# Optimization experiments

Hardware: AMD Instinct MI355X
Metric: run time of the kernel (lower is better)

## Reference

```python
import jax, jax.numpy as jnp
import numpy as np

NUM_HEADS = 16
D_K = 64
D_V = 64
D_MODEL = 1024


def setup_inputs() -> dict:
    key = jax.random.key(0)
    ks = jax.random.split(key, 11)
    B, S = 2, 2048
    s = 0.02
    return {
        "Q": jax.random.normal(ks[0], (B, S, D_MODEL), jnp.float32),
        "K": jax.random.normal(ks[1], (B, S, D_MODEL), jnp.float32),
        "V": jax.random.normal(ks[2], (B, S, D_MODEL), jnp.float32),
        "WQ": jax.random.normal(ks[3], (D_MODEL, NUM_HEADS * D_K), jnp.float32) * s,
        "bQ": jnp.zeros((NUM_HEADS * D_K,), jnp.float32),
        "WK": jax.random.normal(ks[4], (D_MODEL, NUM_HEADS * D_K), jnp.float32) * s,
        "bK": jnp.zeros((NUM_HEADS * D_K,), jnp.float32),
        "WV": jax.random.normal(ks[5], (D_MODEL, NUM_HEADS * D_V), jnp.float32) * s,
        "bV": jnp.zeros((NUM_HEADS * D_V,), jnp.float32),
        "WO": jax.random.normal(ks[6], (NUM_HEADS * D_V, D_MODEL), jnp.float32) * s,
        "bO": jnp.zeros((D_MODEL,), jnp.float32),
    }


def reference(Q, K, V, WQ, bQ, WK, bK, WV, bV, WO, bO):
    B = Q.shape[0]
    # linear projections, then split heads: [B, H, S, d]
    q = (Q @ WQ + bQ).reshape(B, -1, NUM_HEADS, D_K).transpose(0, 2, 1, 3)
    k = (K @ WK + bK).reshape(B, -1, NUM_HEADS, D_K).transpose(0, 2, 1, 3)
    v = (V @ WV + bV).reshape(B, -1, NUM_HEADS, D_V).transpose(0, 2, 1, 3)
    # unfused attention: full [B, H, Sq, Sk] score matrix
    scores = jnp.einsum("bhqd,bhkd->bhqk", q, k) / jnp.sqrt(jnp.float32(D_K))
    attn = jax.nn.softmax(scores, axis=-1)  # dropout is identity in eval mode
    out = jnp.einsum("bhqk,bhkd->bhqd", attn, v)
    out = out.transpose(0, 2, 1, 3).reshape(B, -1, NUM_HEADS * D_V)
    return out @ WO + bO
```

## Files before the change

### kernel.cpp

```cpp
#include <hip/hip_runtime.h>
#include <hip/hip_bf16.h>
#include <stdint.h>

#define BATCH 2
#define SEQ   2048
#define NH    16
#define DH    64
#define DM    1024
#define MR    (BATCH * SEQ)

typedef __bf16 bf16_t;
typedef bf16_t bf16x4 __attribute__((ext_vector_type(4)));
typedef bf16_t bf16x8 __attribute__((ext_vector_type(8)));
typedef float  f32x4  __attribute__((ext_vector_type(4)));

typedef const __attribute__((address_space(1))) void* gas_t;
typedef       __attribute__((address_space(3))) void* las_t;

__device__ __forceinline__ void gload16(const void* g, void* l) {
  __builtin_amdgcn_global_load_lds((gas_t)g, (las_t)l, 16, 0, 0);
}

__device__ __forceinline__ float fast_exp2(float x) {
#if __has_builtin(__builtin_amdgcn_exp2f)
  return __builtin_amdgcn_exp2f(x);
#else
  float r; asm volatile("v_exp_f32 %0, %1\n\ts_nop 1" : "=v"(r) : "v"(x)); return r;
#endif
}

__global__ __launch_bounds__(256) void cvt3_kernel(const float* __restrict__ x0,
                                                   const float* __restrict__ x1,
                                                   const float* __restrict__ x2,
                                                   bf16_t* __restrict__ y0,
                                                   bf16_t* __restrict__ y1,
                                                   bf16_t* __restrict__ y2, int n) {
  const int z = blockIdx.y;
  const float* x = z == 0 ? x0 : (z == 1 ? x1 : x2);
  bf16_t*      y = z == 0 ? y0 : (z == 1 ? y1 : y2);
  int i = (blockIdx.x * 256 + threadIdx.x) * 8;
  if (i + 8 <= n) {
    float4 a = *(const float4*)(x + i);
    float4 b = *(const float4*)(x + i + 4);
    bf16x8 o;
    o[0] = (bf16_t)a.x; o[1] = (bf16_t)a.y; o[2] = (bf16_t)a.z; o[3] = (bf16_t)a.w;
    o[4] = (bf16_t)b.x; o[5] = (bf16_t)b.y; o[6] = (bf16_t)b.z; o[7] = (bf16_t)b.w;
    *(bf16x8*)(y + i) = o;
  }
}

__global__ __launch_bounds__(256) void wtrans4_kernel(const float* __restrict__ W0,
                                                      const float* __restrict__ W1,
                                                      const float* __restrict__ W2,
                                                      const float* __restrict__ W3,
                                                      bf16_t* __restrict__ T0,
                                                      bf16_t* __restrict__ T1,
                                                      bf16_t* __restrict__ T2,
                                                      bf16_t* __restrict__ T3) {
  const int z = blockIdx.z;
  const float* W = z == 0 ? W0 : (z == 1 ? W1 : (z == 2 ? W2 : W3));
  bf16_t*     Wt = z == 0 ? T0 : (z == 1 ? T1 : (z == 2 ? T2 : T3));
  __shared__ bf16_t t[64][65];
  const int c0 = blockIdx.x * 64, r0 = blockIdx.y * 64;
  const int tid = threadIdx.x;
  const int r = tid >> 2, cc = (tid & 3) * 16;
  const float* src = W + (size_t)(r0 + r) * DM + c0 + cc;
#pragma unroll
  for (int i = 0; i < 16; ++i) t[r][cc + i] = (bf16_t)src[i];
  __syncthreads();
  bf16_t* dst = Wt + (size_t)(c0 + r) * DM + r0 + cc;
#pragma unroll
  for (int i = 0; i < 16; ++i) dst[i] = t[cc + i][r];
}

__global__ __launch_bounds__(256) void vtrans_kernel(const bf16_t* __restrict__ v,
                                                     bf16_t* __restrict__ vT) {
  __shared__ bf16_t t[64][65];
  const int s0 = blockIdx.x * 64;
  const int h = blockIdx.y, b = blockIdx.z;
  const int tid = threadIdx.x;
  const int r = tid >> 2, cc = (tid & 3) * 16;
  const bf16_t* src = v + (size_t)(b * SEQ + s0 + r) * DM + h * DH + cc;
#pragma unroll
  for (int i = 0; i < 16; ++i) t[r][cc + i] = src[i];
  __syncthreads();
  bf16_t* dst = vT + (size_t)((b * NH + h) * DH + r) * SEQ + s0 + cc;
#pragma unroll
  for (int i = 0; i < 16; ++i) dst[i] = t[cc + i][r];
}

__global__ __launch_bounds__(256) void gemm3_kernel(
    const bf16_t* __restrict__ A0, const bf16_t* __restrict__ A1,
    const bf16_t* __restrict__ A2,
    const bf16_t* __restrict__ B0, const bf16_t* __restrict__ B1,
    const bf16_t* __restrict__ B2,
    const float* __restrict__ bi0, const float* __restrict__ bi1,
    const float* __restrict__ bi2,
    float s0, float s1, float s2,
    bf16_t* __restrict__ C0, bf16_t* __restrict__ C1, bf16_t* __restrict__ C2) {
  const int z = blockIdx.z;
  const bf16_t* A    = z == 0 ? A0 : (z == 1 ? A1 : A2);
  const bf16_t* Bt   = z == 0 ? B0 : (z == 1 ? B1 : B2);
  const float*  bias = z == 0 ? bi0 : (z == 1 ? bi1 : bi2);
  const float   scale = z == 0 ? s0 : (z == 1 ? s1 : s2);
  bf16_t*       C    = z == 0 ? C0 : (z == 1 ? C1 : C2);
  const int K = DM, N = DM;

  __shared__ __attribute__((aligned(16))) bf16_t As[128 * 64];
  __shared__ __attribute__((aligned(16))) bf16_t Bs[128 * 64];
  const int m0 = blockIdx.x * 128, n0 = blockIdx.y * 128;
  const int tid = threadIdx.x;
  const int wave = tid >> 6, lane = tid & 63;
  const int lm = lane & 15, lg = lane >> 4;
  const int wr = wave >> 1, wc = wave & 1;
  f32x4 acc[4][4];
#pragma unroll
  for (int a = 0; a < 4; ++a)
#pragma unroll
    for (int bb = 0; bb < 4; ++bb) acc[a][bb] = (f32x4){0.f, 0.f, 0.f, 0.f};

  for (int k0 = 0; k0 < K; k0 += 64) {
    __syncthreads();
#pragma unroll
    for (int i = 0; i < 4; ++i) {
      const int c = tid + i * 256;
      const int row = c >> 3, j = c & 7, js = j ^ (row & 7);
      gload16(A  + (size_t)(m0 + row) * K + k0 + js * 8,
              As + (size_t)(wave * 64 + i * 256) * 8);
      gload16(Bt + (size_t)(n0 + row) * K + k0 + js * 8,
              Bs + (size_t)(wave * 64 + i * 256) * 8);
    }
    asm volatile("s_waitcnt vmcnt(0)" ::: "memory");
    __syncthreads();
#pragma unroll
    for (int kk = 0; kk < 2; ++kk) {
      bf16x8 af[4], bfr[4];
#pragma unroll
      for (int t = 0; t < 4; ++t) {
        const int ra = wr * 64 + t * 16 + lm;
        af[t] = *(const bf16x8*)((const char*)As + ra * 128 +
                                 ((kk * 64 + lg * 16) ^ ((ra & 7) << 4)));
        const int rb = wc * 64 + t * 16 + lm;
        bfr[t] = *(const bf16x8*)((const char*)Bs + rb * 128 +
                                  ((kk * 64 + lg * 16) ^ ((rb & 7) << 4)));
      }
      __builtin_amdgcn_s_setprio(1);
#pragma unroll
      for (int mf = 0; mf < 4; ++mf)
#pragma unroll
        for (int nf = 0; nf < 4; ++nf)
          acc[mf][nf] = __builtin_amdgcn_mfma_f32_16x16x32_bf16(af[mf], bfr[nf],
                                                                acc[mf][nf], 0, 0, 0);
      __builtin_amdgcn_s_setprio(0);
    }
  }
#pragma unroll
  for (int mf = 0; mf < 4; ++mf)
#pragma unroll
    for (int nf = 0; nf < 4; ++nf) {
      const int col = n0 + wc * 64 + nf * 16 + lm;
      const float bv = bias[col];
#pragma unroll
      for (int i = 0; i < 4; ++i) {
        const int row = m0 + wr * 64 + mf * 16 + lg * 4 + i;
        C[(size_t)row * N + col] = (bf16_t)((acc[mf][nf][i] + bv) * scale);
      }
    }
}

template <int OUT_BF16>
__global__ __launch_bounds__(256) void gemm_kernel(const bf16_t* __restrict__ A,
                                                   const bf16_t* __restrict__ Bt,
                                                   const float* __restrict__ bias,
                                                   float scale,
                                                   void* __restrict__ Cv,
                                                   int K, int N) {
  __shared__ __attribute__((aligned(16))) bf16_t As[64 * 64];
  __shared__ __attribute__((aligned(16))) bf16_t Bs[128 * 64];
  const int m0 = blockIdx.x * 64, n0 = blockIdx.y * 128;
  const int tid = threadIdx.x;
  const int wave = tid >> 6, lane = tid & 63;
  const int lm = lane & 15, lg = lane >> 4;
  const int wr = wave >> 1, wc = wave & 1;
  f32x4 acc[2][4];
#pragma unroll
  for (int a = 0; a < 2; ++a)
#pragma unroll
    for (int bb = 0; bb < 4; ++bb) acc[a][bb] = (f32x4){0.f, 0.f, 0.f, 0.f};

  for (int k0 = 0; k0 < K; k0 += 64) {
    __syncthreads();
#pragma unroll
    for (int i = 0; i < 2; ++i) {
      const int c = tid + i * 256;
      const int row = c >> 3, j = c & 7, js = j ^ (row & 7);
      gload16(A + (size_t)(m0 + row) * K + k0 + js * 8,
              As + (size_t)(wave * 64 + i * 256) * 8);
    }
#pragma unroll
    for (int i = 0; i < 4; ++i) {
      const int c = tid + i * 256;
      const int row = c >> 3, j = c & 7, js = j ^ (row & 7);
      gload16(Bt + (size_t)(n0 + row) * K + k0 + js * 8,
              Bs + (size_t)(wave * 64 + i * 256) * 8);
    }
    asm volatile("s_waitcnt vmcnt(0)" ::: "memory");
    __syncthreads();
#pragma unroll
    for (int kk = 0; kk < 2; ++kk) {
      bf16x8 af[2], bfr[4];
#pragma unroll
      for (int t = 0; t < 2; ++t) {
        const int ra = wr * 32 + t * 16 + lm;
        af[t] = *(const bf16x8*)((const char*)As + ra * 128 +
                                 ((kk * 64 + lg * 16) ^ ((ra & 7) << 4)));
      }
#pragma unroll
      for (int t = 0; t < 4; ++t) {
        const int rb = wc * 64 + t * 16 + lm;
        bfr[t] = *(const bf16x8*)((const char*)Bs + rb * 128 +
                                  ((kk * 64 + lg * 16) ^ ((rb & 7) << 4)));
      }
      __builtin_amdgcn_s_setprio(1);
#pragma unroll
      for (int mf = 0; mf < 2; ++mf)
#pragma unroll
        for (int nf = 0; nf < 4; ++nf)
          acc[mf][nf] = __builtin_amdgcn_mfma_f32_16x16x32_bf16(af[mf], bfr[nf],
                                                                acc[mf][nf], 0, 0, 0);
      __builtin_amdgcn_s_setprio(0);
    }
  }
#pragma unroll
  for (int mf = 0; mf < 2; ++mf)
#pragma unroll
    for (int nf = 0; nf < 4; ++nf) {
      const int col = n0 + wc * 64 + nf * 16 + lm;
      const float bv = bias[col];
#pragma unroll
      for (int i = 0; i < 4; ++i) {
        const int row = m0 + wr * 32 + mf * 16 + lg * 4 + i;
        const float val = (acc[mf][nf][i] + bv) * scale;
        if (OUT_BF16) ((bf16_t*)Cv)[(size_t)row * N + col] = (bf16_t)val;
        else          ((float*)Cv)[(size_t)row * N + col] = val;
      }
    }
}

__global__ __launch_bounds__(512, 4) void flash_kernel(const bf16_t* __restrict__ q,
                                                       const bf16_t* __restrict__ k,
                                                       const bf16_t* __restrict__ vT,
                                                       bf16_t* __restrict__ o) {
  __shared__ __attribute__((aligned(16))) bf16_t Ks[2][64 * 64];
  __shared__ __attribute__((aligned(16))) bf16_t Vs[2][64 * 64];
  __shared__ __attribute__((aligned(16))) bf16_t Ps[8][16 * 64];
  const int wg = blockIdx.x;
  const int swz = (wg & 7) * 64 + (wg >> 3);
  const int qt = swz & 15, h = (swz >> 4) & 15, b = swz >> 8;
  const int tid = threadIdx.x;
  const int wave = tid >> 6, lane = tid & 63;
  const int lm = lane & 15, lg = lane >> 4;
  char* PsW = (char*)(&Ps[wave][0]);

  const bf16_t* qb = q + (size_t)(b * SEQ + qt * 128 + wave * 16) * DM + h * DH;
  const int srow = tid >> 3, sjs = (tid & 7) ^ (srow & 7);
  const bf16_t* ksrc = k + (size_t)b * SEQ * DM + h * DH + (size_t)srow * DM + sjs * 8;
  const bf16_t* vsrc = vT + (size_t)(b * NH + h) * DH * SEQ + (size_t)srow * SEQ + sjs * 8;
  bf16_t* kdst0 = &Ks[0][wave * 512];
  bf16_t* kdst1 = &Ks[1][wave * 512];
  bf16_t* vdst0 = &Vs[0][wave * 512];
  bf16_t* vdst1 = &Vs[1][wave * 512];

  bf16x8 qf[2];
#pragma unroll
  for (int kk = 0; kk < 2; ++kk)
    qf[kk] = *(const bf16x8*)(qb + (size_t)lm * DM + kk * 32 + lg * 8);

  f32x4 acc[4];
#pragma unroll
  for (int nf = 0; nf < 4; ++nf) acc[nf] = (f32x4){0.f, 0.f, 0.f, 0.f};
  float mrun = -1e30f, lrun = 0.f;

  gload16(ksrc, kdst0);
  gload16(vsrc, vdst0);

  const int NT = SEQ / 64;
  for (int t = 0; t < NT; ++t) {
    const int cur = t & 1;
    asm volatile("" ::: "memory");
    __builtin_amdgcn_s_barrier();
    if (t + 1 < NT) {
      gload16(ksrc + (size_t)(t + 1) * 64 * DM, cur ? kdst0 : kdst1);
      gload16(vsrc + (t + 1) * 64,              cur ? vdst0 : vdst1);
      asm volatile("s_waitcnt vmcnt(2)" ::: "memory");
    } else {
      asm volatile("s_waitcnt vmcnt(0)" ::: "memory");
    }
    __builtin_amdgcn_s_barrier();
    asm volatile("" ::: "memory");

    const char* Kb_ = (const char*)&Ks[cur][0];
    const char* Vb_ = (const char*)&Vs[cur][0];

    bf16x8 kf[2][4];
#pragma unroll
    for (int kk = 0; kk < 2; ++kk)
#pragma unroll
      for (int nf = 0; nf < 4; ++nf) {
        const int row = nf * 16 + lm;
        kf[kk][nf] = *(const bf16x8*)(Kb_ + row * 128 +
                                      ((kk * 64 + lg * 16) ^ ((row & 7) << 4)));
      }
    f32x4 sc[4];
#pragma unroll
    for (int nf = 0; nf < 4; ++nf) sc[nf] = (f32x4){0.f, 0.f, 0.f, 0.f};
    __builtin_amdgcn_s_setprio(1);
#pragma unroll
    for (int kk = 0; kk < 2; ++kk)
#pragma unroll
      for (int nf = 0; nf < 4; ++nf)
        sc[nf] = __builtin_amdgcn_mfma_f32_16x16x32_bf16(kf[kk][nf], qf[kk],
                                                         sc[nf], 0, 0, 0);
    __builtin_amdgcn_s_setprio(0);

    float ml = fmaxf(
        fmaxf(fmaxf(fmaxf(sc[0][0], sc[0][1]), fmaxf(sc[0][2], sc[0][3])),
              fmaxf(fmaxf(sc[1][0], sc[1][1]), fmaxf(sc[1][2], sc[1][3]))),
        fmaxf(fmaxf(fmaxf(sc[2][0], sc[2][1]), fmaxf(sc[2][2], sc[2][3])),
              fmaxf(fmaxf(sc[3][0], sc[3][1]), fmaxf(sc[3][2], sc[3][3]))));
    ml = fmaxf(ml, __shfl_xor(ml, 16));
    ml = fmaxf(ml, __shfl_xor(ml, 32));
    const bool defer = __all(ml - mrun <= 8.0f);
    const float mn = defer ? mrun : fmaxf(mrun, ml);
#pragma unroll
    for (int nf = 0; nf < 4; ++nf)
#pragma unroll
      for (int i = 0; i < 4; ++i) sc[nf][i] = fast_exp2(sc[nf][i] - mn);
    float s = ((sc[0][0] + sc[0][1]) + (sc[0][2] + sc[0][3])) +
              ((sc[1][0] + sc[1][1]) + (sc[1][2] + sc[1][3])) +
              ((sc[2][0] + sc[2][1]) + (sc[2][2] + sc[2][3])) +
              ((sc[3][0] + sc[3][1]) + (sc[3][2] + sc[3][3]));
    s += __shfl_xor(s, 16);
    s += __shfl_xor(s, 32);
    if (defer) {
      lrun += s;
    } else {
      const float alpha = fast_exp2(mrun - mn);
      mrun = mn;
      lrun = lrun * alpha + s;
      float ai[4];
#pragma unroll
      for (int i = 0; i < 4; ++i) ai[i] = __shfl(alpha, (lane & 48) | (lg * 4 + i));
#pragma unroll
      for (int nf = 0; nf < 4; ++nf)
#pragma unroll
        for (int i = 0; i < 4; ++i) acc[nf][i] *= ai[i];
    }

#pragma unroll
    for (int nf = 0; nf < 4; ++nf) {
      bf16x4 pw;
      pw[0] = (bf16_t)sc[nf][0]; pw[1] = (bf16_t)sc[nf][1];
      pw[2] = (bf16_t)sc[nf][2]; pw[3] = (bf16_t)sc[nf][3];
      *(bf16x4*)(PsW + lm * 128 + ((nf * 32 + lg * 8) ^ ((lm & 7) << 4))) = pw;
    }

#pragma unroll
    for (int kk = 0; kk < 2; ++kk) {
      bf16x8 pf = *(const bf16x8*)(PsW + lm * 128 +
                                   ((kk * 64 + lg * 16) ^ ((lm & 7) << 4)));
      bf16x8 vf[4];
#pragma unroll
      for (int nf = 0; nf < 4; ++nf) {
        const int row = nf * 16 + lm;
        vf[nf] = *(const bf16x8*)(Vb_ + row * 128 +
                                  ((kk * 64 + lg * 16) ^ ((row & 7) << 4)));
      }
      __builtin_amdgcn_s_setprio(1);
#pragma unroll
      for (int nf = 0; nf < 4; ++nf)
        acc[nf] = __builtin_amdgcn_mfma_f32_16x16x32_bf16(pf, vf[nf],
                                                          acc[nf], 0, 0, 0);
      __builtin_amdgcn_s_setprio(0);
    }
  }

  const float inv = __builtin_amdgcn_rcpf(lrun);
  float li[4];
#pragma unroll
  for (int i = 0; i < 4; ++i) li[i] = __shfl(inv, (lane & 48) | (lg * 4 + i));
#pragma unroll
  for (int i = 0; i < 4; ++i) {
    const int row = b * SEQ + qt * 128 + wave * 16 + lg * 4 + i;
#pragma unroll
    for (int nf = 0; nf < 4; ++nf) {
      const int col = h * DH + nf * 16 + lm;
      o[(size_t)row * DM + col] = (bf16_t)(acc[nf][i] * li[i]);
    }
  }
}

extern "C" void kernel_launch(void* const* d_in, const int* in_sizes, int n_in,
                              void* d_out, int out_size, void* d_ws, size_t ws_size,
                              hipStream_t stream) {
  (void)in_sizes; (void)n_in; (void)out_size; (void)ws_size;
  const float* Q  = (const float*)d_in[0];
  const float* Kx = (const float*)d_in[1];
  const float* V  = (const float*)d_in[2];
  const float* WQ = (const float*)d_in[3];
  const float* bQ = (const float*)d_in[4];
  const float* WK = (const float*)d_in[5];
  const float* bK = (const float*)d_in[6];
  const float* WV = (const float*)d_in[7];
  const float* bV = (const float*)d_in[8];
  const float* WO = (const float*)d_in[9];
  const float* bO = (const float*)d_in[10];

  const size_t MS  = (size_t)MR * DM;
  const size_t WSZ = (size_t)DM * DM;
  bf16_t* ws  = (bf16_t*)d_ws;
  bf16_t* Qb  = ws;
  bf16_t* Kb  = Qb + MS;
  bf16_t* Vb  = Kb + MS;
  bf16_t* WQt = Vb + MS;
  bf16_t* WKt = WQt + WSZ;
  bf16_t* WVt = WKt + WSZ;
  bf16_t* WOt = WVt + WSZ;
  bf16_t* qp  = WOt + WSZ;
  bf16_t* kp  = qp + MS;
  bf16_t* vp  = kp + MS;
  bf16_t* vTb = Qb;
  bf16_t* ao  = Kb;

  const float scale_q = 0.125f * 1.44269504088896340736f;

  cvt3_kernel<<<dim3((unsigned)(MS / 2048), 3), 256, 0, stream>>>(Q, Kx, V, Qb, Kb, Vb, (int)MS);
  wtrans4_kernel<<<dim3(16, 16, 4), 256, 0, stream>>>(WQ, WK, WV, WO, WQt, WKt, WVt, WOt);

  gemm3_kernel<<<dim3(32, 8, 3), 256, 0, stream>>>(Qb, Kb, Vb,
                                                   WQt, WKt, WVt,
                                                   bQ, bK, bV,
                                                   scale_q, 1.0f, 1.0f,
                                                   qp, kp, vp);

  vtrans_kernel<<<dim3(SEQ / 64, NH, BATCH), 256, 0, stream>>>(vp, vTb);
  flash_kernel<<<dim3(512), 512, 0, stream>>>(qp, kp, vTb, ao);
  gemm_kernel<0><<<dim3(MR / 64, DM / 128), 256, 0, stream>>>(ao, WOt, bO, 1.0f, d_out, DM, DM);
}
```

Before: 138.1 us.

## Switch flash attention to 32x32x16 MFMA with 32-row waves, 4 waves/block

Rewrites the flash attention kernel so each wave handles 32 query rows using 32x32x16 bf16 MFMA instead of 16x16x32. Blocks shrink from 8 to 4 waves, each thread issues two K/V global-to-LDS loads per tile, and the softmax row reductions and rescale shuffles are adapted to the 32x32 accumulator layout. The aim is fewer MFMA instructions and LDS fragment reads per unit of work, since each K/V fragment is reused across more query rows. The cost is more accumulator registers per wave and fewer waves per block, which may lower occupancy and latency hiding.

New measurement: 138.6 us. Within noise of the previous version (+0.3%).

```diff
diff --git a/kernel.cpp b/kernel.cpp
--- a/kernel.cpp
+++ b/kernel.cpp
@@ -13,6 +13,7 @@
 typedef bf16_t bf16x4 __attribute__((ext_vector_type(4)));
 typedef bf16_t bf16x8 __attribute__((ext_vector_type(8)));
 typedef float  f32x4  __attribute__((ext_vector_type(4)));
+typedef float  f32x16 __attribute__((ext_vector_type(16)));
 
 typedef const __attribute__((address_space(1))) void* gas_t;
 typedef       __attribute__((address_space(3))) void* las_t;
@@ -247,42 +248,45 @@
     }
 }
 
-__global__ __launch_bounds__(512, 4) void flash_kernel(const bf16_t* __restrict__ q,
+__global__ __launch_bounds__(256, 3) void flash_kernel(const bf16_t* __restrict__ q,
                                                        const bf16_t* __restrict__ k,
                                                        const bf16_t* __restrict__ vT,
                                                        bf16_t* __restrict__ o) {
   __shared__ __attribute__((aligned(16))) bf16_t Ks[2][64 * 64];
   __shared__ __attribute__((aligned(16))) bf16_t Vs[2][64 * 64];
-  __shared__ __attribute__((aligned(16))) bf16_t Ps[8][16 * 64];
+  __shared__ __attribute__((aligned(16))) bf16_t Ps[4][32 * 64];
   const int wg = blockIdx.x;
   const int swz = (wg & 7) * 64 + (wg >> 3);
   const int qt = swz & 15, h = (swz >> 4) & 15, b = swz >> 8;
   const int tid = threadIdx.x;
   const int wave = tid >> 6, lane = tid & 63;
-  const int lm = lane & 15, lg = lane >> 4;
+  const int lq = lane & 31, hi = lane >> 5;
   char* PsW = (char*)(&Ps[wave][0]);
 
-  const bf16_t* qb = q + (size_t)(b * SEQ + qt * 128 + wave * 16) * DM + h * DH;
-  const int srow = tid >> 3, sjs = (tid & 7) ^ (srow & 7);
-  const bf16_t* ksrc = k + (size_t)b * SEQ * DM + h * DH + (size_t)srow * DM + sjs * 8;
-  const bf16_t* vsrc = vT + (size_t)(b * NH + h) * DH * SEQ + (size_t)srow * SEQ + sjs * 8;
-  bf16_t* kdst0 = &Ks[0][wave * 512];
-  bf16_t* kdst1 = &Ks[1][wave * 512];
-  bf16_t* vdst0 = &Vs[0][wave * 512];
-  bf16_t* vdst1 = &Vs[1][wave * 512];
-
-  bf16x8 qf[2];
-#pragma unroll
-  for (int kk = 0; kk < 2; ++kk)
-    qf[kk] = *(const bf16x8*)(qb + (size_t)lm * DM + kk * 32 + lg * 8);
-
-  f32x4 acc[4];
-#pragma unroll
-  for (int nf = 0; nf < 4; ++nf) acc[nf] = (f32x4){0.f, 0.f, 0.f, 0.f};
+  const bf16_t* qb = q + (size_t)(b * SEQ + qt * 128 + wave * 32) * DM + h * DH;
+  const int c0r = tid >> 3,  c0j = (tid & 7) ^ (c0r & 7);
+  const int c1r = c0r + 32,  c1j = (tid & 7) ^ (c1r & 7);
+  const bf16_t* kbase = k + (size_t)b * SEQ * DM + h * DH;
+  const bf16_t* vbase = vT + (size_t)(b * NH + h) * DH * SEQ;
+  const bf16_t* ks0 = kbase + (size_t)c0r * DM + c0j * 8;
+  const bf16_t* ks1 = kbase + (size_t)c1r * DM + c1j * 8;
+  const bf16_t* vs0 = vbase + (size_t)c0r * SEQ + c0j * 8;
+  const bf16_t* vs1 = vbase + (size_t)c1r * SEQ + c1j * 8;
+
+  bf16x8 qf[4];
+#pragma unroll
+  for (int ds = 0; ds < 4; ++ds)
+    qf[ds] = *(const bf16x8*)(qb + (size_t)lq * DM + ds * 16 + hi * 8);
+
+  f32x16 acc[2];
+#pragma unroll
+  for (int r = 0; r < 16; ++r) { acc[0][r] = 0.f; acc[1][r] = 0.f; }
   float mrun = -1e30f, lrun = 0.f;
 
-  gload16(ksrc, kdst0);
-  gload16(vsrc, vdst0);
+  gload16(ks0, &Ks[0][(wave * 64) * 8]);
+  gload16(ks1, &Ks[0][(wave * 64 + 256) * 8]);
+  gload16(vs0, &Vs[0][(wave * 64) * 8]);
+  gload16(vs1, &Vs[0][(wave * 64 + 256) * 8]);
 
   const int NT = SEQ / 64;
   for (int t = 0; t < NT; ++t) {
@@ -290,9 +294,12 @@
     asm volatile("" ::: "memory");
     __builtin_amdgcn_s_barrier();
     if (t + 1 < NT) {
-      gload16(ksrc + (size_t)(t + 1) * 64 * DM, cur ? kdst0 : kdst1);
-      gload16(vsrc + (t + 1) * 64,              cur ? vdst0 : vdst1);
-      asm volatile("s_waitcnt vmcnt(2)" ::: "memory");
+      const int nb = cur ^ 1;
+      gload16(ks0 + (size_t)(t + 1) * 64 * DM, &Ks[nb][(wave * 64) * 8]);
+      gload16(ks1 + (size_t)(t + 1) * 64 * DM, &Ks[nb][(wave * 64 + 256) * 8]);
+      gload16(vs0 + (t + 1) * 64,              &Vs[nb][(wave * 64) * 8]);
+      gload16(vs1 + (t + 1) * 64,              &Vs[nb][(wave * 64 + 256) * 8]);
+      asm volatile("s_waitcnt vmcnt(4)" ::: "memory");
     } else {
       asm volatile("s_waitcnt vmcnt(0)" ::: "memory");
     }
@@ -302,45 +309,37 @@
     const char* Kb_ = (const char*)&Ks[cur][0];
     const char* Vb_ = (const char*)&Vs[cur][0];
 
-    bf16x8 kf[2][4];
-#pragma unroll
-    for (int kk = 0; kk < 2; ++kk)
-#pragma unroll
-      for (int nf = 0; nf < 4; ++nf) {
-        const int row = nf * 16 + lm;
-        kf[kk][nf] = *(const bf16x8*)(Kb_ + row * 128 +
-                                      ((kk * 64 + lg * 16) ^ ((row & 7) << 4)));
-      }
-    f32x4 sc[4];
-#pragma unroll
-    for (int nf = 0; nf < 4; ++nf) sc[nf] = (f32x4){0.f, 0.f, 0.f, 0.f};
+    f32x16 sc[2];
+#pragma unroll
+    for (int r = 0; r < 16; ++r) { sc[0][r] = 0.f; sc[1][r] = 0.f; }
     __builtin_amdgcn_s_setprio(1);
 #pragma unroll
-    for (int kk = 0; kk < 2; ++kk)
-#pragma unroll
-      for (int nf = 0; nf < 4; ++nf)
-        sc[nf] = __builtin_amdgcn_mfma_f32_16x16x32_bf16(kf[kk][nf], qf[kk],
-                                                         sc[nf], 0, 0, 0);
+    for (int ds = 0; ds < 4; ++ds) {
+#pragma unroll
+      for (int kt = 0; kt < 2; ++kt) {
+        const int row = kt * 32 + lq;
+        bf16x8 kfrag = *(const bf16x8*)(Kb_ + row * 128 +
+                                        ((ds * 32 + hi * 16) ^ ((row & 7) << 4)));
+        sc[kt] = __builtin_amdgcn_mfma_f32_32x32x16_bf16(kfrag, qf[ds], sc[kt], 0, 0, 0);
+      }
+    }
     __builtin_amdgcn_s_setprio(0);
 
-    float ml = fmaxf(
-        fmaxf(fmaxf(fmaxf(sc[0][0], sc[0][1]), fmaxf(sc[0][2], sc[0][3])),
-              fmaxf(fmaxf(sc[1][0], sc[1][1]), fmaxf(sc[1][2], sc[1][3]))),
-        fmaxf(fmaxf(fmaxf(sc[2][0], sc[2][1]), fmaxf(sc[2][2], sc[2][3])),
-              fmaxf(fmaxf(sc[3][0], sc[3][1]), fmaxf(sc[3][2], sc[3][3]))));
-    ml = fmaxf(ml, __shfl_xor(ml, 16));
+    float ml = sc[0][0];
+#pragma unroll
+    for (int r = 1; r < 16; ++r) ml = fmaxf(ml, sc[0][r]);
+#pragma unroll
+    for (int r = 0; r < 16; ++r) ml = fmaxf(ml, sc[1][r]);
     ml = fmaxf(ml, __shfl_xor(ml, 32));
     const bool defer = __all(ml - mrun <= 8.0f);
     const float mn = defer ? mrun : fmaxf(mrun, ml);
 #pragma unroll
-    for (int nf = 0; nf < 4; ++nf)
-#pragma unroll
-      for (int i = 0; i < 4; ++i) sc[nf][i] = fast_exp2(sc[nf][i] - mn);
-    float s = ((sc[0][0] + sc[0][1]) + (sc[0][2] + sc[0][3])) +
-              ((sc[1][0] + sc[1][1]) + (sc[1][2] + sc[1][3])) +
-              ((sc[2][0] + sc[2][1]) + (sc[2][2] + sc[2][3])) +
-              ((sc[3][0] + sc[3][1]) + (sc[3][2] + sc[3][3]));
-    s += __shfl_xor(s, 16);
+    for (int kt = 0; kt < 2; ++kt)
+#pragma unroll
+      for (int r = 0; r < 16; ++r) sc[kt][r] = fast_exp2(sc[kt][r] - mn);
+    float s = 0.f;
+#pragma unroll
+    for (int r = 0; r < 16; ++r) s += sc[0][r] + sc[1][r];
     s += __shfl_xor(s, 32);
     if (defer) {
       lrun += s;
@@ -348,54 +347,51 @@
       const float alpha = fast_exp2(mrun - mn);
       mrun = mn;
       lrun = lrun * alpha + s;
-      float ai[4];
-#pragma unroll
-      for (int i = 0; i < 4; ++i) ai[i] = __shfl(alpha, (lane & 48) | (lg * 4 + i));
-#pragma unroll
-      for (int nf = 0; nf < 4; ++nf)
-#pragma unroll
-        for (int i = 0; i < 4; ++i) acc[nf][i] *= ai[i];
-    }
-
-#pragma unroll
-    for (int nf = 0; nf < 4; ++nf) {
-      bf16x4 pw;
-      pw[0] = (bf16_t)sc[nf][0]; pw[1] = (bf16_t)sc[nf][1];
-      pw[2] = (bf16_t)sc[nf][2]; pw[3] = (bf16_t)sc[nf][3];
-      *(bf16x4*)(PsW + lm * 128 + ((nf * 32 + lg * 8) ^ ((lm & 7) << 4))) = pw;
-    }
-
-#pragma unroll
-    for (int kk = 0; kk < 2; ++kk) {
-      bf16x8 pf = *(const bf16x8*)(PsW + lm * 128 +
-                                   ((kk * 64 + lg * 16) ^ ((lm & 7) << 4)));
-      bf16x8 vf[4];
-#pragma unroll
-      for (int nf = 0; nf < 4; ++nf) {
-        const int row = nf * 16 + lm;
-        vf[nf] = *(const bf16x8*)(Vb_ + row * 128 +
-                                  ((kk * 64 + lg * 16) ^ ((row & 7) << 4)));
-      }
+#pragma unroll
+      for (int r = 0; r < 16; ++r) {
+        const float ar = __shfl(alpha, (r & 3) + 8 * (r >> 2) + 4 * hi);
+        acc[0][r] *= ar;
+        acc[1][r] *= ar;
+      }
+    }
+
+#pragma unroll
+    for (int kt = 0; kt < 2; ++kt)
+#pragma unroll
+      for (int g = 0; g < 4; ++g) {
+        bf16x4 pw;
+        pw[0] = (bf16_t)sc[kt][4 * g + 0]; pw[1] = (bf16_t)sc[kt][4 * g + 1];
+        pw[2] = (bf16_t)sc[kt][4 * g + 2]; pw[3] = (bf16_t)sc[kt][4 * g + 3];
+        *(bf16x4*)(PsW + lq * 128 +
+                   ((kt * 64 + g * 16 + hi * 8) ^ ((lq & 7) << 4))) = pw;
+      }
+
+#pragma unroll
+    for (int ks = 0; ks < 4; ++ks) {
+      bf16x8 pf = *(const bf16x8*)(PsW + lq * 128 +
+                                   ((ks * 32 + hi * 16) ^ ((lq & 7) << 4)));
       __builtin_amdgcn_s_setprio(1);
 #pragma unroll
-      for (int nf = 0; nf < 4; ++nf)
-        acc[nf] = __builtin_amdgcn_mfma_f32_16x16x32_bf16(pf, vf[nf],
-                                                          acc[nf], 0, 0, 0);
+      for (int dt = 0; dt < 2; ++dt) {
+        const int row = dt * 32 + lq;
+        bf16x8 vfrag = *(const bf16x8*)(Vb_ + row * 128 +
+                                        ((ks * 32 + hi * 16) ^ ((row & 7) << 4)));
+        acc[dt] = __builtin_amdgcn_mfma_f32_32x32x16_bf16(pf, vfrag, acc[dt], 0, 0, 0);
+      }
       __builtin_amdgcn_s_setprio(0);
     }
   }
 
   const float inv = __builtin_amdgcn_rcpf(lrun);
-  float li[4];
-#pragma unroll
-  for (int i = 0; i < 4; ++i) li[i] = __shfl(inv, (lane & 48) | (lg * 4 + i));
-#pragma unroll
-  for (int i = 0; i < 4; ++i) {
-    const int row = b * SEQ + qt * 128 + wave * 16 + lg * 4 + i;
-#pragma unroll
-    for (int nf = 0; nf < 4; ++nf) {
-      const int col = h * DH + nf * 16 + lm;
-      o[(size_t)row * DM + col] = (bf16_t)(acc[nf][i] * li[i]);
+#pragma unroll
+  for (int r = 0; r < 16; ++r) {
+    const int qrow = (r & 3) + 8 * (r >> 2) + 4 * hi;
+    const float iv = __shfl(inv, qrow);
+    const int row = b * SEQ + qt * 128 + wave * 32 + qrow;
+#pragma unroll
+    for (int dt = 0; dt < 2; ++dt) {
+      const int col = h * DH + dt * 32 + lq;
+      o[(size_t)row * DM + col] = (bf16_t)(acc[dt][r] * iv);
     }
   }
 }
@@ -444,6 +440,6 @@
                                                    qp, kp, vp);
 
   vtrans_kernel<<<dim3(SEQ / 64, NH, BATCH), 256, 0, stream>>>(vp, vTb);
-  flash_kernel<<<dim3(512), 512, 0, stream>>>(qp, kp, vTb, ao);
+  flash_kernel<<<dim3(512), 256, 0, stream>>>(qp, kp, vTb, ao);
   gemm_kernel<0><<<dim3(MR / 64, DM / 128), 256, 0, stream>>>(ao, WOt, bO, 1.0f, d_out, DM, DM);
 }
```
